# Optimization experiments

Measured on AMD Instinct MI355X. Metric: run time of the kernel, lower is better.

The kernel has to match this reference:

```python
import jax, jax.numpy as jnp
import numpy as np

N = 50000      # nodes
E = 800000     # edges (before self loops)
IN_DIM = 128
HID = 16
HEADS = 8
OUT_DIM = 40
NEG_SLOPE = 0.2


def setup_inputs() -> dict:
    key = jax.random.key(0)
    ks = jax.random.split(key, 10)
    x = jax.random.normal(ks[0], (N, IN_DIM), jnp.float32)
    edge_index = jax.random.randint(ks[1], (2, E), 0, N, dtype=jnp.int32)
    # layer 1: GATConv(IN_DIM, HID, heads=HEADS, concat=True)
    W1 = jax.random.normal(ks[2], (IN_DIM, HEADS * HID), jnp.float32) / np.sqrt(IN_DIM).astype(np.float32)
    att_src1 = jax.random.normal(ks[3], (HEADS, HID), jnp.float32) * 0.1
    att_dst1 = jax.random.normal(ks[4], (HEADS, HID), jnp.float32) * 0.1
    bias1 = jnp.zeros((HEADS * HID,), jnp.float32)
    # layer 2: GATConv(HEADS*HID, OUT_DIM, heads=1, concat=False)
    W2 = jax.random.normal(ks[5], (HEADS * HID, OUT_DIM), jnp.float32) / np.sqrt(HEADS * HID).astype(np.float32)
    att_src2 = jax.random.normal(ks[6], (1, OUT_DIM), jnp.float32) * 0.1
    att_dst2 = jax.random.normal(ks[7], (1, OUT_DIM), jnp.float32) * 0.1
    bias2 = jnp.zeros((OUT_DIM,), jnp.float32)
    return {"x": x, "W1": W1, "att_src1": att_src1, "att_dst1": att_dst1, "bias1": bias1,
            "W2": W2, "att_src2": att_src2, "att_dst2": att_dst2, "bias2": bias2,
            "edge_index": edge_index}


def gat_conv(x, src, dst, W, att_src, att_dst, bias, heads, dim, concat, num_nodes):
    # h: [N, H, D]
    h = (x @ W).reshape(num_nodes, heads, dim)
    a_src = jnp.sum(h * att_src, axis=-1)  # [N, H]
    a_dst = jnp.sum(h * att_dst, axis=-1)  # [N, H]
    e = a_src[src] + a_dst[dst]            # [E', H]
    e = jnp.where(e > 0, e, NEG_SLOPE * e)  # leaky_relu
    # segment softmax over edges sharing the same target node
    m = jax.ops.segment_max(e, dst, num_segments=num_nodes)  # [N, H]
    e = jnp.exp(e - m[dst])
    s = jax.ops.segment_sum(e, dst, num_segments=num_nodes)  # [N, H]
    alpha = e / (s[dst] + 1e-16)            # [E', H]
    msg = h[src] * alpha[:, :, None]        # [E', H, D]
    out = jax.ops.segment_sum(msg, dst, num_segments=num_nodes)  # [N, H, D]
    if concat:
        out = out.reshape(num_nodes, heads * dim)
    else:
        out = out.mean(axis=1)
    return out + bias


def reference(x, W1, att_src1, att_dst1, bias1, W2, att_src2, att_dst2, bias2, edge_index):
    # add self loops (PyG GATConv default)
    loop = jnp.arange(N, dtype=edge_index.dtype)
    src = jnp.concatenate([edge_index[0], loop])
    dst = jnp.concatenate([edge_index[1], loop])
    # eval mode: dropout (p=0.6) is identity
    h = gat_conv(x, src, dst, W1, att_src1, att_dst1, bias1, HEADS, HID, True, N)
    h = jax.nn.elu(h)
    out = gat_conv(h, src, dst, W2, att_src2, att_dst2, bias2, 1, OUT_DIM, False, N)
    return jax.nn.log_softmax(out, axis=1)
```

## Files before the change

kernel.cpp:

```cpp
#include <hip/hip_runtime.h>
#include <math.h>

#define IN_DIM 128
#define HEADS 8
#define HID 16
#define OUT_DIM 40
#define NEG 0.2f

typedef short bf16x8 __attribute__((ext_vector_type(8)));
typedef float f32x4 __attribute__((ext_vector_type(4)));

__device__ __forceinline__ unsigned short f32_to_bf16_rne(float v) {
  unsigned u = __float_as_uint(v);
  return (unsigned short)((u + 0x7FFFu + ((u >> 16) & 1u)) >> 16);
}


__global__ void zero_ints(int* p, int n) {
  int i = blockIdx.x * blockDim.x + threadIdx.x;
  if (i < n) p[i] = 0;
}

__global__ void hist_k(const int* __restrict__ ei, int E0, int N, int* __restrict__ deg) {
  int e = blockIdx.x * blockDim.x + threadIdx.x;
  int EP = E0 + N;
  if (e >= EP) return;
  int d = (e < E0) ? ei[E0 + e] : (e - E0);
  atomicAdd(&deg[d], 1);
}

__global__ __launch_bounds__(1024) void scanA_k(const int* __restrict__ deg, int* __restrict__ rp,
                                                int* __restrict__ bsum, int n) {
  __shared__ int wsum[16];
  int tid = threadIdx.x;
  int i = blockIdx.x * 1024 + tid;
  int lane = tid & 63, w = tid >> 6;
  int v = (i < n) ? deg[i] : 0;
  int x = v;
  #pragma unroll
  for (int off = 1; off < 64; off <<= 1) {
    int y = __shfl_up(x, off);
    if (lane >= off) x += y;
  }
  if (lane == 63) wsum[w] = x;
  __syncthreads();
  if (tid < 16) {
    int s = wsum[tid];
    #pragma unroll
    for (int off = 1; off < 16; off <<= 1) {
      int y = __shfl_up(s, off);
      if (tid >= off) s += y;
    }
    wsum[tid] = s;
  }
  __syncthreads();
  int woff = (w == 0) ? 0 : wsum[w - 1];
  if (i < n) rp[i] = woff + x - v;
  if (tid == 0) bsum[blockIdx.x] = wsum[15];
}

__global__ __launch_bounds__(1024) void scanB_k(int* __restrict__ bsum, int nb,
                                                int* __restrict__ rp, int n) {
  __shared__ int wsum[16];
  int tid = threadIdx.x;
  int lane = tid & 63, w = tid >> 6;
  int v = (tid < nb) ? bsum[tid] : 0;
  int x = v;
  #pragma unroll
  for (int off = 1; off < 64; off <<= 1) {
    int y = __shfl_up(x, off);
    if (lane >= off) x += y;
  }
  if (lane == 63) wsum[w] = x;
  __syncthreads();
  if (tid < 16) {
    int s = wsum[tid];
    #pragma unroll
    for (int off = 1; off < 16; off <<= 1) {
      int y = __shfl_up(s, off);
      if (tid >= off) s += y;
    }
    wsum[tid] = s;
  }
  __syncthreads();
  int woff = (w == 0) ? 0 : wsum[w - 1];
  if (tid < nb) bsum[tid] = woff + x - v;
  if (tid == 0) rp[n] = wsum[15];
}

__global__ __launch_bounds__(1024) void scanC_k(int* __restrict__ rp, const int* __restrict__ bsum,
                                                int* __restrict__ cnt, int n) {
  int i = blockIdx.x * 1024 + threadIdx.x;
  if (i < n) {
    int v = rp[i] + bsum[blockIdx.x];
    rp[i] = v;
    cnt[i] = v;
  }
}

__global__ void scatter_k(const int* __restrict__ ei, int E0, int N,
                          int* __restrict__ cnt, int* __restrict__ csr_src) {
  int e = blockIdx.x * blockDim.x + threadIdx.x;
  int EP = E0 + N;
  if (e >= EP) return;
  int s, d;
  if (e < E0) { s = ei[e]; d = ei[E0 + e]; } else { s = e - E0; d = s; }
  int pos = atomicAdd(&cnt[d], 1);
  csr_src[pos] = s;
}

__global__ void prep_w1_k(const float* __restrict__ W1, const float* __restrict__ as1,
                          const float* __restrict__ ad1,
                          unsigned short* __restrict__ whi, unsigned short* __restrict__ wlo) {
  int t = blockIdx.x * 256 + threadIdx.x;
  if (t >= 9 * 4 * 64 * 8) return;
  int j = t & 7, lane = (t >> 3) & 63, kc = (t >> 9) & 3, ct = t >> 11;
  int k = kc * 32 + (lane >> 4) * 8 + j;
  int col = lane & 15;
  float v;
  if (ct < 8) {
    v = W1[k * 128 + ct * 16 + col];
  } else {
    int h = col & 7;
    const float* att = (col < 8) ? as1 : ad1;
    float s = 0.f;
    #pragma unroll
    for (int d = 0; d < 16; ++d) s += W1[k * 128 + h * 16 + d] * att[h * 16 + d];
    v = s;
  }
  unsigned u = __float_as_uint(v);
  unsigned hi = (u + 0x7FFFu + ((u >> 16) & 1u)) >> 16;
  float rem = v - __uint_as_float(hi << 16);
  unsigned ur = __float_as_uint(rem);
  unsigned lo = (ur + 0x7FFFu + ((ur >> 16) & 1u)) >> 16;
  whi[t] = (unsigned short)hi;
  wlo[t] = (unsigned short)lo;
}

__global__ __launch_bounds__(256) void gemm1_mfma_k(
    const float* __restrict__ x, const unsigned short* __restrict__ whi,
    const unsigned short* __restrict__ wlo,
    unsigned short* __restrict__ h1, float* __restrict__ a1s, float* __restrict__ a1d, int N) {
  int w = threadIdx.x >> 6, lane = threadIdx.x & 63;
  int quad = lane >> 4, l15 = lane & 15;
  int row = blockIdx.x * 64 + w * 16 + l15;
  int rowc = (row < N) ? row : (N - 1);

  f32x4 acc[9];
  #pragma unroll
  for (int t = 0; t < 9; ++t) acc[t] = (f32x4){0.f, 0.f, 0.f, 0.f};

  const float* xr = x + (size_t)rowc * 128 + quad * 8;
  #pragma unroll
  for (int kc = 0; kc < 4; ++kc) {
    f32x4 a0 = *reinterpret_cast<const f32x4*>(xr + kc * 32);
    f32x4 a1 = *reinterpret_cast<const f32x4*>(xr + kc * 32 + 4);
    float av[8] = {a0.x, a0.y, a0.z, a0.w, a1.x, a1.y, a1.z, a1.w};
    bf16x8 ahi, alo;
    #pragma unroll
    for (int j = 0; j < 8; ++j) {
      unsigned u = __float_as_uint(av[j]);
      unsigned hi = (u + 0x7FFFu + ((u >> 16) & 1u)) >> 16;
      float rem = av[j] - __uint_as_float(hi << 16);
      unsigned ur = __float_as_uint(rem);
      unsigned lo = (ur + 0x7FFFu + ((ur >> 16) & 1u)) >> 16;
      ahi[j] = (short)hi;
      alo[j] = (short)lo;
    }
    #pragma unroll
    for (int ct = 0; ct < 9; ++ct) {
      bf16x8 bh = *reinterpret_cast<const bf16x8*>(whi + ((size_t)(ct * 4 + kc) * 64 + lane) * 8);
      bf16x8 bl = *reinterpret_cast<const bf16x8*>(wlo + ((size_t)(ct * 4 + kc) * 64 + lane) * 8);
      acc[ct] = __builtin_amdgcn_mfma_f32_16x16x32_bf16(ahi, bh, acc[ct], 0, 0, 0);
      acc[ct] = __builtin_amdgcn_mfma_f32_16x16x32_bf16(ahi, bl, acc[ct], 0, 0, 0);
      acc[ct] = __builtin_amdgcn_mfma_f32_16x16x32_bf16(alo, bh, acc[ct], 0, 0, 0);
    }
  }
  int rbase = blockIdx.x * 64 + w * 16 + quad * 4;
  #pragma unroll
  for (int reg = 0; reg < 4; ++reg) {
    int r = rbase + reg;
    if (r < N) {
      #pragma unroll
      for (int ct = 0; ct < 8; ++ct)
        h1[(size_t)r * 128 + ct * 16 + l15] = f32_to_bf16_rne(acc[ct][reg]);
      float v = acc[8][reg];
      if (l15 < 8) a1s[r * 8 + l15] = v;
      else         a1d[r * 8 + (l15 - 8)] = v;
    }
  }
}

__global__ __launch_bounds__(256) void agg1_k(
    const int* __restrict__ row_ptr, const int* __restrict__ csr_src,
    const float* __restrict__ a1s, const float* __restrict__ a1d,
    const unsigned* __restrict__ h1u, const float* __restrict__ bias1,
    const float* __restrict__ W2, const float* __restrict__ att_s2, const float* __restrict__ att_d2,
    unsigned short* __restrict__ h2, float* __restrict__ a2s, float* __restrict__ a2d, int N) {
  int wid = threadIdx.x >> 6;
  int lane = threadIdx.x & 63;
  int n = blockIdx.x * 4 + wid;
  if (n >= N) return;

  __shared__ float vrow_s[4][128];
  float* vrow = vrow_s[wid];

  int rs = row_ptr[n], re = row_ptr[n + 1];
  int h = lane >> 3;
  float adn = a1d[n * 8 + h];

  float accx = 0.f, accy = 0.f, sw = 0.f;
  int i = rs;
  for (; i + 4 <= re; i += 4) {
    int s0 = csr_src[i], s1 = csr_src[i + 1], s2 = csr_src[i + 2], s3 = csr_src[i + 3];
    float e0 = a1s[s0 * 8 + h] + adn;
    float e1 = a1s[s1 * 8 + h] + adn;
    float e2 = a1s[s2 * 8 + h] + adn;
    float e3 = a1s[s3 * 8 + h] + adn;
    unsigned u0 = h1u[(size_t)s0 * 64 + lane];
    unsigned u1 = h1u[(size_t)s1 * 64 + lane];
    unsigned u2 = h1u[(size_t)s2 * 64 + lane];
    unsigned u3 = h1u[(size_t)s3 * 64 + lane];
    e0 = (e0 > 0.f) ? e0 : NEG * e0;
    e1 = (e1 > 0.f) ? e1 : NEG * e1;
    e2 = (e2 > 0.f) ? e2 : NEG * e2;
    e3 = (e3 > 0.f) ? e3 : NEG * e3;
    float w0 = __expf(e0), w1 = __expf(e1), w2 = __expf(e2), w3 = __expf(e3);
    sw += (w0 + w1) + (w2 + w3);
    accx += w0 * __uint_as_float(u0 << 16) + w1 * __uint_as_float(u1 << 16)
          + w2 * __uint_as_float(u2 << 16) + w3 * __uint_as_float(u3 << 16);
    accy += w0 * __uint_as_float(u0 & 0xFFFF0000u) + w1 * __uint_as_float(u1 & 0xFFFF0000u)
          + w2 * __uint_as_float(u2 & 0xFFFF0000u) + w3 * __uint_as_float(u3 & 0xFFFF0000u);
  }
  for (; i < re; ++i) {
    int s = csr_src[i];
    float e = a1s[s * 8 + h] + adn;
    e = (e > 0.f) ? e : NEG * e;
    float w = __expf(e);
    unsigned u = h1u[(size_t)s * 64 + lane];
    sw += w;
    accx += w * __uint_as_float(u << 16);
    accy += w * __uint_as_float(u & 0xFFFF0000u);
  }
  float inv = 1.f / (sw + 1e-16f);
  float2 b = *reinterpret_cast<const float2*>(bias1 + 2 * lane);
  float vx = accx * inv + b.x;
  float vy = accy * inv + b.y;
  vx = (vx > 0.f) ? vx : (__expf(vx) - 1.f);
  vy = (vy > 0.f) ? vy : (__expf(vy) - 1.f);
  vrow[2 * lane] = vx;
  vrow[2 * lane + 1] = vy;

  float hacc = 0.f;
  int c = lane;
  if (c < OUT_DIM) {
    #pragma unroll 4
    for (int k = 0; k < 128; k += 4) {
      float4 vk = *reinterpret_cast<const float4*>(vrow + k);
      hacc += vk.x * W2[k * OUT_DIM + c] + vk.y * W2[(k + 1) * OUT_DIM + c]
            + vk.z * W2[(k + 2) * OUT_DIM + c] + vk.w * W2[(k + 3) * OUT_DIM + c];
    }
    h2[(size_t)n * OUT_DIM + c] = f32_to_bf16_rne(hacc);
  }
  float vs = (c < OUT_DIM) ? hacc * att_s2[c] : 0.f;
  float vd = (c < OUT_DIM) ? hacc * att_d2[c] : 0.f;
  #pragma unroll
  for (int off = 32; off > 0; off >>= 1) {
    vs += __shfl_xor(vs, off);
    vd += __shfl_xor(vd, off);
  }
  if (lane == 0) { a2s[n] = vs; a2d[n] = vd; }
}

__global__ __launch_bounds__(256) void agg2_k(
    const int* __restrict__ row_ptr, const int* __restrict__ csr_src,
    const float* __restrict__ a2s, const float* __restrict__ a2d,
    const unsigned short* __restrict__ h2, const float* __restrict__ bias2,
    float* __restrict__ out, int N) {
  int wid = threadIdx.x >> 6;
  int lane = threadIdx.x & 63;
  int n = blockIdx.x * 4 + wid;
  if (n >= N) return;

  int rs = row_ptr[n], re = row_ptr[n + 1];
  float adn = a2d[n];
  bool act = lane < OUT_DIM;
  int c = act ? lane : 0;
  float acc = 0.f, sw = 0.f;
  int i = rs;
  for (; i + 4 <= re; i += 4) {
    int s0 = csr_src[i], s1 = csr_src[i + 1], s2 = csr_src[i + 2], s3 = csr_src[i + 3];
    float e0 = a2s[s0] + adn, e1 = a2s[s1] + adn, e2 = a2s[s2] + adn, e3 = a2s[s3] + adn;
    unsigned g0 = h2[(size_t)s0 * OUT_DIM + c];
    unsigned g1 = h2[(size_t)s1 * OUT_DIM + c];
    unsigned g2 = h2[(size_t)s2 * OUT_DIM + c];
    unsigned g3 = h2[(size_t)s3 * OUT_DIM + c];
    e0 = (e0 > 0.f) ? e0 : NEG * e0;
    e1 = (e1 > 0.f) ? e1 : NEG * e1;
    e2 = (e2 > 0.f) ? e2 : NEG * e2;
    e3 = (e3 > 0.f) ? e3 : NEG * e3;
    float w0 = __expf(e0), w1 = __expf(e1), w2 = __expf(e2), w3 = __expf(e3);
    sw += (w0 + w1) + (w2 + w3);
    acc += w0 * __uint_as_float(g0 << 16) + w1 * __uint_as_float(g1 << 16)
         + w2 * __uint_as_float(g2 << 16) + w3 * __uint_as_float(g3 << 16);
  }
  for (; i < re; ++i) {
    int s = csr_src[i];
    float e = a2s[s] + adn;
    e = (e > 0.f) ? e : NEG * e;
    float w = __expf(e);
    sw += w;
    unsigned g = h2[(size_t)s * OUT_DIM + c];
    acc += w * __uint_as_float(g << 16);
  }
  float v = act ? (acc / (sw + 1e-16f) + bias2[c]) : -1e30f;
  float vm = v;
  #pragma unroll
  for (int off = 32; off > 0; off >>= 1) vm = fmaxf(vm, __shfl_xor(vm, off));
  float ex = act ? __expf(v - vm) : 0.f;
  float es = ex;
  #pragma unroll
  for (int off = 32; off > 0; off >>= 1) es += __shfl_xor(es, off);
  if (act) out[(size_t)n * OUT_DIM + c] = v - vm - __logf(es);
}


extern "C" void kernel_launch(void* const* d_in, const int* in_sizes, int n_in,
                              void* d_out, int out_size, void* d_ws, size_t ws_size,
                              hipStream_t stream) {
  const float* x   = (const float*)d_in[0];
  const float* W1  = (const float*)d_in[1];
  const float* as1 = (const float*)d_in[2];
  const float* ad1 = (const float*)d_in[3];
  const float* b1  = (const float*)d_in[4];
  const float* W2  = (const float*)d_in[5];
  const float* as2 = (const float*)d_in[6];
  const float* ad2 = (const float*)d_in[7];
  const float* b2  = (const float*)d_in[8];
  const int*   ei  = (const int*)d_in[9];
  int N  = in_sizes[0] / IN_DIM;
  int E0 = in_sizes[9] / 2;
  int EP = E0 + N;
  float* out = (float*)d_out;

  char* ws = (char*)d_ws;
  size_t off = 0;
  auto alloc = [&](size_t bytes) {
    char* p = ws + off;
    off += (bytes + 255) & ~size_t(255);
    return p;
  };
  unsigned short* h1 = (unsigned short*)alloc((size_t)N * 128 * 2);
  float* a1s  = (float*)alloc((size_t)N * 8 * 4);
  float* a1d  = (float*)alloc((size_t)N * 8 * 4);
  unsigned short* h2 = (unsigned short*)alloc((size_t)N * 40 * 2);
  float* a2s  = (float*)alloc((size_t)N * 4);
  float* a2d  = (float*)alloc((size_t)N * 4);
  int*   deg  = (int*)alloc((size_t)N * 4);
  int*   cnt  = (int*)alloc((size_t)N * 4);
  int*   rp   = (int*)alloc((size_t)(N + 4) * 4);
  int*   bsum = (int*)alloc((size_t)1024 * 4);
  int*   csr  = (int*)alloc((size_t)EP * 4);
  unsigned short* whi = (unsigned short*)alloc((size_t)9 * 4 * 64 * 8 * 2);
  unsigned short* wlo = (unsigned short*)alloc((size_t)9 * 4 * 64 * 8 * 2);

  int nb = (N + 1023) / 1024;
  zero_ints<<<(N + 255) / 256, 256, 0, stream>>>(deg, N);
  hist_k<<<(EP + 255) / 256, 256, 0, stream>>>(ei, E0, N, deg);
  scanA_k<<<nb, 1024, 0, stream>>>(deg, rp, bsum, N);
  scanB_k<<<1, 1024, 0, stream>>>(bsum, nb, rp, N);
  scanC_k<<<nb, 1024, 0, stream>>>(rp, bsum, cnt, N);
  scatter_k<<<(EP + 255) / 256, 256, 0, stream>>>(ei, E0, N, cnt, csr);
  prep_w1_k<<<(9 * 4 * 64 * 8 + 255) / 256, 256, 0, stream>>>(W1, as1, ad1, whi, wlo);
  gemm1_mfma_k<<<(N + 63) / 64, 256, 0, stream>>>(x, whi, wlo, h1, a1s, a1d, N);
  agg1_k<<<(N + 3) / 4, 256, 0, stream>>>(rp, csr, a1s, a1d, (const unsigned*)h1, b1, W2, as2, ad2, h2, a2s, a2d, N);
  agg2_k<<<(N + 3) / 4, 256, 0, stream>>>(rp, csr, a2s, a2d, h2, b2, out, N);
}
```

Baseline: 316.9 us.

## Compute edge weights cooperatively across lanes and broadcast via readlane/shuffle

```diff
diff --git a/kernel.cpp b/kernel.cpp
--- a/kernel.cpp
+++ b/kernel.cpp
@@ -206,43 +206,35 @@
   float* vrow = vrow_s[wid];
 
   int rs = row_ptr[n], re = row_ptr[n + 1];
-  int h = lane >> 3;
-  float adn = a1d[n * 8 + h];
-
-  float accx = 0.f, accy = 0.f, sw = 0.f;
-  int i = rs;
-  for (; i + 4 <= re; i += 4) {
-    int s0 = csr_src[i], s1 = csr_src[i + 1], s2 = csr_src[i + 2], s3 = csr_src[i + 3];
-    float e0 = a1s[s0 * 8 + h] + adn;
-    float e1 = a1s[s1 * 8 + h] + adn;
-    float e2 = a1s[s2 * 8 + h] + adn;
-    float e3 = a1s[s3 * 8 + h] + adn;
-    unsigned u0 = h1u[(size_t)s0 * 64 + lane];
-    unsigned u1 = h1u[(size_t)s1 * 64 + lane];
-    unsigned u2 = h1u[(size_t)s2 * 64 + lane];
-    unsigned u3 = h1u[(size_t)s3 * 64 + lane];
-    e0 = (e0 > 0.f) ? e0 : NEG * e0;
-    e1 = (e1 > 0.f) ? e1 : NEG * e1;
-    e2 = (e2 > 0.f) ? e2 : NEG * e2;
-    e3 = (e3 > 0.f) ? e3 : NEG * e3;
-    float w0 = __expf(e0), w1 = __expf(e1), w2 = __expf(e2), w3 = __expf(e3);
-    sw += (w0 + w1) + (w2 + w3);
-    accx += w0 * __uint_as_float(u0 << 16) + w1 * __uint_as_float(u1 << 16)
-          + w2 * __uint_as_float(u2 << 16) + w3 * __uint_as_float(u3 << 16);
-    accy += w0 * __uint_as_float(u0 & 0xFFFF0000u) + w1 * __uint_as_float(u1 & 0xFFFF0000u)
-          + w2 * __uint_as_float(u2 & 0xFFFF0000u) + w3 * __uint_as_float(u3 & 0xFFFF0000u);
-  }
-  for (; i < re; ++i) {
-    int s = csr_src[i];
-    float e = a1s[s * 8 + h] + adn;
-    e = (e > 0.f) ? e : NEG * e;
-    float w = __expf(e);
-    unsigned u = h1u[(size_t)s * 64 + lane];
-    sw += w;
-    accx += w * __uint_as_float(u << 16);
-    accy += w * __uint_as_float(u & 0xFFFF0000u);
-  }
-  float inv = 1.f / (sw + 1e-16f);
+  int jslot = lane >> 3;
+  int hw = lane & 7;
+  int head = lane >> 3;
+  float adn = a1d[n * 8 + hw];
+
+  float accx = 0.f, accy = 0.f, sww = 0.f;
+  for (int i0 = rs; i0 < re; i0 += 8) {
+    int idx = i0 + jslot;
+    int sj = csr_src[idx < re ? idx : re - 1];
+    float e = a1s[sj * 8 + hw] + adn;
+    e = fmaxf(e, NEG * e);
+    float w = (idx < re) ? __expf(e) : 0.f;
+    sww += w;
+    #pragma unroll
+    for (int jj = 0; jj < 8; ++jj) {
+      if (i0 + jj >= re) break;
+      int s_u = __builtin_amdgcn_readlane(sj, jj * 8);
+      float w_b = __shfl(w, jj * 8 + head);
+      unsigned u = h1u[(size_t)s_u * 64 + lane];
+      accx += w_b * __uint_as_float(u << 16);
+      accy += w_b * __uint_as_float(u & 0xFFFF0000u);
+    }
+  }
+  sww += __shfl_xor(sww, 8);
+  sww += __shfl_xor(sww, 16);
+  sww += __shfl_xor(sww, 32);
+  float swh = __shfl(sww, head);
+
+  float inv = 1.f / (swh + 1e-16f);
   float2 b = *reinterpret_cast<const float2*>(bias1 + 2 * lane);
   float vx = accx * inv + b.x;
   float vy = accy * inv + b.y;
@@ -286,34 +278,27 @@
   float adn = a2d[n];
   bool act = lane < OUT_DIM;
   int c = act ? lane : 0;
-  float acc = 0.f, sw = 0.f;
-  int i = rs;
-  for (; i + 4 <= re; i += 4) {
-    int s0 = csr_src[i], s1 = csr_src[i + 1], s2 = csr_src[i + 2], s3 = csr_src[i + 3];
-    float e0 = a2s[s0] + adn, e1 = a2s[s1] + adn, e2 = a2s[s2] + adn, e3 = a2s[s3] + adn;
-    unsigned g0 = h2[(size_t)s0 * OUT_DIM + c];
-    unsigned g1 = h2[(size_t)s1 * OUT_DIM + c];
-    unsigned g2 = h2[(size_t)s2 * OUT_DIM + c];
-    unsigned g3 = h2[(size_t)s3 * OUT_DIM + c];
-    e0 = (e0 > 0.f) ? e0 : NEG * e0;
-    e1 = (e1 > 0.f) ? e1 : NEG * e1;
-    e2 = (e2 > 0.f) ? e2 : NEG * e2;
-    e3 = (e3 > 0.f) ? e3 : NEG * e3;
-    float w0 = __expf(e0), w1 = __expf(e1), w2 = __expf(e2), w3 = __expf(e3);
-    sw += (w0 + w1) + (w2 + w3);
-    acc += w0 * __uint_as_float(g0 << 16) + w1 * __uint_as_float(g1 << 16)
-         + w2 * __uint_as_float(g2 << 16) + w3 * __uint_as_float(g3 << 16);
-  }
-  for (; i < re; ++i) {
-    int s = csr_src[i];
-    float e = a2s[s] + adn;
-    e = (e > 0.f) ? e : NEG * e;
-    float w = __expf(e);
-    sw += w;
-    unsigned g = h2[(size_t)s * OUT_DIM + c];
-    acc += w * __uint_as_float(g << 16);
-  }
-  float v = act ? (acc / (sw + 1e-16f) + bias2[c]) : -1e30f;
+  float acc = 0.f, swl = 0.f;
+  for (int i0 = rs; i0 < re; i0 += 64) {
+    int idx = i0 + lane;
+    int sL = csr_src[idx < re ? idx : re - 1];
+    float e = a2s[sL] + adn;
+    e = fmaxf(e, NEG * e);
+    float w = (idx < re) ? __expf(e) : 0.f;
+    swl += w;
+    int m = re - i0; if (m > 64) m = 64;
+    #pragma unroll 4
+    for (int jj = 0; jj < m; ++jj) {
+      int s_u = __builtin_amdgcn_readlane(sL, jj);
+      float w_u = __shfl(w, jj);
+      unsigned g = h2[(size_t)s_u * OUT_DIM + c];
+      acc += w_u * __uint_as_float(g << 16);
+    }
+  }
+  #pragma unroll
+  for (int off = 32; off > 0; off >>= 1) swl += __shfl_xor(swl, off);
+
+  float v = act ? (acc / (swl + 1e-16f) + bias2[c]) : -1e30f;
   float vm = v;
   #pragma unroll
   for (int off = 32; off > 0; off >>= 1) vm = fmaxf(vm, __shfl_xor(vm, off));
```

After: 342.4 us. 8.0% more time.

## Fold deg zeroing and W2 prep into one kernel, pad h2 rows, transpose W2

Applied to the files above, without the earlier changes.

```diff
diff --git a/kernel.cpp b/kernel.cpp
--- a/kernel.cpp
+++ b/kernel.cpp
@@ -15,11 +15,6 @@
   return (unsigned short)((u + 0x7FFFu + ((u >> 16) & 1u)) >> 16);
 }
 
-
-__global__ void zero_ints(int* p, int n) {
-  int i = blockIdx.x * blockDim.x + threadIdx.x;
-  if (i < n) p[i] = 0;
-}
 
 __global__ void hist_k(const int* __restrict__ ei, int E0, int N, int* __restrict__ deg) {
   int e = blockIdx.x * blockDim.x + threadIdx.x;
@@ -109,32 +104,50 @@
   csr_src[pos] = s;
 }
 
-__global__ void prep_w1_k(const float* __restrict__ W1, const float* __restrict__ as1,
-                          const float* __restrict__ ad1,
-                          unsigned short* __restrict__ whi, unsigned short* __restrict__ wlo) {
+__global__ void prep_k(const float* __restrict__ W1, const float* __restrict__ as1,
+                       const float* __restrict__ ad1, const float* __restrict__ W2,
+                       const float* __restrict__ as2, const float* __restrict__ ad2,
+                       unsigned short* __restrict__ whi, unsigned short* __restrict__ wlo,
+                       float* __restrict__ W2T, int* __restrict__ deg, int N) {
   int t = blockIdx.x * 256 + threadIdx.x;
-  if (t >= 9 * 4 * 64 * 8) return;
-  int j = t & 7, lane = (t >> 3) & 63, kc = (t >> 9) & 3, ct = t >> 11;
-  int k = kc * 32 + (lane >> 4) * 8 + j;
-  int col = lane & 15;
-  float v;
-  if (ct < 8) {
-    v = W1[k * 128 + ct * 16 + col];
-  } else {
-    int h = col & 7;
-    const float* att = (col < 8) ? as1 : ad1;
-    float s = 0.f;
-    #pragma unroll
-    for (int d = 0; d < 16; ++d) s += W1[k * 128 + h * 16 + d] * att[h * 16 + d];
-    v = s;
-  }
-  unsigned u = __float_as_uint(v);
-  unsigned hi = (u + 0x7FFFu + ((u >> 16) & 1u)) >> 16;
-  float rem = v - __uint_as_float(hi << 16);
-  unsigned ur = __float_as_uint(rem);
-  unsigned lo = (ur + 0x7FFFu + ((ur >> 16) & 1u)) >> 16;
-  whi[t] = (unsigned short)hi;
-  wlo[t] = (unsigned short)lo;
+  if (t < N) deg[t] = 0;
+  if (t < 18432) {
+    int j = t & 7, lane = (t >> 3) & 63, kc = (t >> 9) & 3, ct = t >> 11;
+    int k = kc * 32 + (lane >> 4) * 8 + j;
+    int col = lane & 15;
+    float v;
+    if (ct < 8) {
+      v = W1[k * 128 + ct * 16 + col];
+    } else {
+      int h = col & 7;
+      const float* att = (col < 8) ? as1 : ad1;
+      float s = 0.f;
+      #pragma unroll
+      for (int d = 0; d < 16; ++d) s += W1[k * 128 + h * 16 + d] * att[h * 16 + d];
+      v = s;
+    }
+    unsigned u = __float_as_uint(v);
+    unsigned hi = (u + 0x7FFFu + ((u >> 16) & 1u)) >> 16;
+    float rem = v - __uint_as_float(hi << 16);
+    unsigned ur = __float_as_uint(rem);
+    unsigned lo = (ur + 0x7FFFu + ((ur >> 16) & 1u)) >> 16;
+    whi[t] = (unsigned short)hi;
+    wlo[t] = (unsigned short)lo;
+  } else if (t < 18432 + 42 * 128) {
+    int t2 = t - 18432;
+    int c = t2 >> 7, k = t2 & 127;
+    float v;
+    if (c < OUT_DIM) {
+      v = W2[k * OUT_DIM + c];
+    } else {
+      const float* att = (c == OUT_DIM) ? as2 : ad2;
+      float s = 0.f;
+      #pragma unroll 8
+      for (int d = 0; d < OUT_DIM; ++d) s += W2[k * OUT_DIM + d] * att[d];
+      v = s;
+    }
+    W2T[c * 128 + k] = v;
+  }
 }
 
 __global__ __launch_bounds__(256) void gemm1_mfma_k(
@@ -195,7 +208,7 @@
     const int* __restrict__ row_ptr, const int* __restrict__ csr_src,
     const float* __restrict__ a1s, const float* __restrict__ a1d,
     const unsigned* __restrict__ h1u, const float* __restrict__ bias1,
-    const float* __restrict__ W2, const float* __restrict__ att_s2, const float* __restrict__ att_d2,
+    const float* __restrict__ W2T,
     unsigned short* __restrict__ h2, float* __restrict__ a2s, float* __restrict__ a2d, int N) {
   int wid = threadIdx.x >> 6;
   int lane = threadIdx.x & 63;
@@ -205,7 +218,8 @@
   __shared__ float vrow_s[4][128];
   float* vrow = vrow_s[wid];
 
-  int rs = row_ptr[n], re = row_ptr[n + 1];
+  int rs = __builtin_amdgcn_readfirstlane(row_ptr[n]);
+  int re = __builtin_amdgcn_readfirstlane(row_ptr[n + 1]);
   int h = lane >> 3;
   float adn = a1d[n * 8 + h];
 
@@ -221,10 +235,10 @@
     unsigned u1 = h1u[(size_t)s1 * 64 + lane];
     unsigned u2 = h1u[(size_t)s2 * 64 + lane];
     unsigned u3 = h1u[(size_t)s3 * 64 + lane];
-    e0 = (e0 > 0.f) ? e0 : NEG * e0;
-    e1 = (e1 > 0.f) ? e1 : NEG * e1;
-    e2 = (e2 > 0.f) ? e2 : NEG * e2;
-    e3 = (e3 > 0.f) ? e3 : NEG * e3;
+    e0 = fmaxf(e0, NEG * e0);
+    e1 = fmaxf(e1, NEG * e1);
+    e2 = fmaxf(e2, NEG * e2);
+    e3 = fmaxf(e3, NEG * e3);
     float w0 = __expf(e0), w1 = __expf(e1), w2 = __expf(e2), w3 = __expf(e3);
     sw += (w0 + w1) + (w2 + w3);
     accx += w0 * __uint_as_float(u0 << 16) + w1 * __uint_as_float(u1 << 16)
@@ -235,7 +249,7 @@
   for (; i < re; ++i) {
     int s = csr_src[i];
     float e = a1s[s * 8 + h] + adn;
-    e = (e > 0.f) ? e : NEG * e;
+    e = fmaxf(e, NEG * e);
     float w = __expf(e);
     unsigned u = h1u[(size_t)s * 64 + lane];
     sw += w;
@@ -251,25 +265,19 @@
   vrow[2 * lane] = vx;
   vrow[2 * lane + 1] = vy;
 
-  float hacc = 0.f;
-  int c = lane;
-  if (c < OUT_DIM) {
-    #pragma unroll 4
+  if (lane < 42) {
+    const float* wrow = W2T + lane * 128;
+    float hacc = 0.f;
+    #pragma unroll 8
     for (int k = 0; k < 128; k += 4) {
       float4 vk = *reinterpret_cast<const float4*>(vrow + k);
-      hacc += vk.x * W2[k * OUT_DIM + c] + vk.y * W2[(k + 1) * OUT_DIM + c]
-            + vk.z * W2[(k + 2) * OUT_DIM + c] + vk.w * W2[(k + 3) * OUT_DIM + c];
-    }
-    h2[(size_t)n * OUT_DIM + c] = f32_to_bf16_rne(hacc);
-  }
-  float vs = (c < OUT_DIM) ? hacc * att_s2[c] : 0.f;
-  float vd = (c < OUT_DIM) ? hacc * att_d2[c] : 0.f;
-  #pragma unroll
-  for (int off = 32; off > 0; off >>= 1) {
-    vs += __shfl_xor(vs, off);
-    vd += __shfl_xor(vd, off);
-  }
-  if (lane == 0) { a2s[n] = vs; a2d[n] = vd; }
+      float4 wk = *reinterpret_cast<const float4*>(wrow + k);
+      hacc += vk.x * wk.x + vk.y * wk.y + vk.z * wk.z + vk.w * wk.w;
+    }
+    if (lane < OUT_DIM)      h2[(size_t)n * 64 + lane] = f32_to_bf16_rne(hacc);
+    else if (lane == OUT_DIM) a2s[n] = hacc;
+    else                      a2d[n] = hacc;
+  }
 }
 
 __global__ __launch_bounds__(256) void agg2_k(
@@ -282,23 +290,23 @@
   int n = blockIdx.x * 4 + wid;
   if (n >= N) return;
 
-  int rs = row_ptr[n], re = row_ptr[n + 1];
+  int rs = __builtin_amdgcn_readfirstlane(row_ptr[n]);
+  int re = __builtin_amdgcn_readfirstlane(row_ptr[n + 1]);
   float adn = a2d[n];
   bool act = lane < OUT_DIM;
-  int c = act ? lane : 0;
   float acc = 0.f, sw = 0.f;
   int i = rs;
   for (; i + 4 <= re; i += 4) {
     int s0 = csr_src[i], s1 = csr_src[i + 1], s2 = csr_src[i + 2], s3 = csr_src[i + 3];
     float e0 = a2s[s0] + adn, e1 = a2s[s1] + adn, e2 = a2s[s2] + adn, e3 = a2s[s3] + adn;
-    unsigned g0 = h2[(size_t)s0 * OUT_DIM + c];
-    unsigned g1 = h2[(size_t)s1 * OUT_DIM + c];
-    unsigned g2 = h2[(size_t)s2 * OUT_DIM + c];
-    unsigned g3 = h2[(size_t)s3 * OUT_DIM + c];
-    e0 = (e0 > 0.f) ? e0 : NEG * e0;
-    e1 = (e1 > 0.f) ? e1 : NEG * e1;
-    e2 = (e2 > 0.f) ? e2 : NEG * e2;
-    e3 = (e3 > 0.f) ? e3 : NEG * e3;
+    unsigned g0 = h2[(size_t)s0 * 64 + lane];
+    unsigned g1 = h2[(size_t)s1 * 64 + lane];
+    unsigned g2 = h2[(size_t)s2 * 64 + lane];
+    unsigned g3 = h2[(size_t)s3 * 64 + lane];
+    e0 = fmaxf(e0, NEG * e0);
+    e1 = fmaxf(e1, NEG * e1);
+    e2 = fmaxf(e2, NEG * e2);
+    e3 = fmaxf(e3, NEG * e3);
     float w0 = __expf(e0), w1 = __expf(e1), w2 = __expf(e2), w3 = __expf(e3);
     sw += (w0 + w1) + (w2 + w3);
     acc += w0 * __uint_as_float(g0 << 16) + w1 * __uint_as_float(g1 << 16)
@@ -307,13 +315,13 @@
   for (; i < re; ++i) {
     int s = csr_src[i];
     float e = a2s[s] + adn;
-    e = (e > 0.f) ? e : NEG * e;
+    e = fmaxf(e, NEG * e);
     float w = __expf(e);
     sw += w;
-    unsigned g = h2[(size_t)s * OUT_DIM + c];
+    unsigned g = h2[(size_t)s * 64 + lane];
     acc += w * __uint_as_float(g << 16);
   }
-  float v = act ? (acc / (sw + 1e-16f) + bias2[c]) : -1e30f;
+  float v = act ? (acc / (sw + 1e-16f) + bias2[lane]) : -1e30f;
   float vm = v;
   #pragma unroll
   for (int off = 32; off > 0; off >>= 1) vm = fmaxf(vm, __shfl_xor(vm, off));
@@ -321,7 +329,7 @@
   float es = ex;
   #pragma unroll
   for (int off = 32; off > 0; off >>= 1) es += __shfl_xor(es, off);
-  if (act) out[(size_t)n * OUT_DIM + c] = v - vm - __logf(es);
+  if (act) out[(size_t)n * OUT_DIM + lane] = v - vm - __logf(es);
 }
 
 
@@ -353,7 +361,7 @@
   unsigned short* h1 = (unsigned short*)alloc((size_t)N * 128 * 2);
   float* a1s  = (float*)alloc((size_t)N * 8 * 4);
   float* a1d  = (float*)alloc((size_t)N * 8 * 4);
-  unsigned short* h2 = (unsigned short*)alloc((size_t)N * 40 * 2);
+  unsigned short* h2 = (unsigned short*)alloc((size_t)N * 64 * 2);
   float* a2s  = (float*)alloc((size_t)N * 4);
   float* a2d  = (float*)alloc((size_t)N * 4);
   int*   deg  = (int*)alloc((size_t)N * 4);
@@ -363,16 +371,17 @@
   int*   csr  = (int*)alloc((size_t)EP * 4);
   unsigned short* whi = (unsigned short*)alloc((size_t)9 * 4 * 64 * 8 * 2);
   unsigned short* wlo = (unsigned short*)alloc((size_t)9 * 4 * 64 * 8 * 2);
+  float* W2T  = (float*)alloc((size_t)42 * 128 * 4);
 
   int nb = (N + 1023) / 1024;
-  zero_ints<<<(N + 255) / 256, 256, 0, stream>>>(deg, N);
+  int prep_n = (N > 18432 + 42 * 128) ? N : (18432 + 42 * 128);
+  prep_k<<<(prep_n + 255) / 256, 256, 0, stream>>>(W1, as1, ad1, W2, as2, ad2, whi, wlo, W2T, deg, N);
   hist_k<<<(EP + 255) / 256, 256, 0, stream>>>(ei, E0, N, deg);
   scanA_k<<<nb, 1024, 0, stream>>>(deg, rp, bsum, N);
   scanB_k<<<1, 1024, 0, stream>>>(bsum, nb, rp, N);
   scanC_k<<<nb, 1024, 0, stream>>>(rp, bsum, cnt, N);
   scatter_k<<<(EP + 255) / 256, 256, 0, stream>>>(ei, E0, N, cnt, csr);
-  prep_w1_k<<<(9 * 4 * 64 * 8 + 255) / 256, 256, 0, stream>>>(W1, as1, ad1, whi, wlo);
   gemm1_mfma_k<<<(N + 63) / 64, 256, 0, stream>>>(x, whi, wlo, h1, a1s, a1d, N);
-  agg1_k<<<(N + 3) / 4, 256, 0, stream>>>(rp, csr, a1s, a1d, (const unsigned*)h1, b1, W2, as2, ad2, h2, a2s, a2d, N);
+  agg1_k<<<(N + 3) / 4, 256, 0, stream>>>(rp, csr, a1s, a1d, (const unsigned*)h1, b1, W2T, h2, a2s, a2d, N);
   agg2_k<<<(N + 3) / 4, 256, 0, stream>>>(rp, csr, a2s, a2d, h2, b2, out, N);
 }
```

Result: slower. 386.1 us (+21.9%).
